# Optimization experiments

Measured on AMD Instinct MI355X. Metric: run time of the kernel, lower is better.

The kernel has to match this reference:

```python
import jax, jax.numpy as jnp
import numpy as np
from jax import lax

DN = ('NCHW', 'OIHW', 'NCHW')

def _bconv(x, w, b):
    # sign-binarized weights, full-precision conv, kernel 3 pad 1 stride 1
    y = lax.conv_general_dilated(x, jnp.sign(w), window_strides=(1, 1),
                                 padding=[(1, 1), (1, 1)], dimension_numbers=DN)
    return y + b[None, :, None, None]

def _maxpool2(x):
    return lax.reduce_window(x, -jnp.inf, lax.max,
                             window_dimensions=(1, 1, 2, 2),
                             window_strides=(1, 1, 2, 2), padding='VALID')

def setup_inputs() -> dict:
    key = jax.random.key(0)
    ks = jax.random.split(key, 11)
    return {
        'x':   jax.random.normal(ks[0], (128, 3, 224, 224), jnp.float32),
        'w1':  jax.random.normal(ks[1], (16, 3, 3, 3), jnp.float32),
        'b1':  jax.random.normal(ks[2], (16,), jnp.float32),
        'w2':  jax.random.normal(ks[3], (32, 16, 3, 3), jnp.float32),
        'b2':  jax.random.normal(ks[4], (32,), jnp.float32),
        'w3':  jax.random.normal(ks[5], (64, 32, 3, 3), jnp.float32),
        'b3':  jax.random.normal(ks[6], (64,), jnp.float32),
        'wf1': jax.random.normal(ks[7], (128, 50176), jnp.float32),
        'bf1': jax.random.normal(ks[8], (128,), jnp.float32),
        'wf2': jax.random.normal(ks[9], (1000, 128), jnp.float32),
        'bf2': jax.random.normal(ks[10], (1000,), jnp.float32),
    }

def reference(x, w1, b1, w2, b2, w3, b3, wf1, bf1, wf2, bf2):
    h = _maxpool2(jax.nn.relu(_bconv(x, w1, b1)))    # [B,16,112,112]
    h = _maxpool2(jax.nn.relu(_bconv(h, w2, b2)))    # [B,32,56,56]
    h = _maxpool2(jax.nn.relu(_bconv(h, w3, b3)))    # [B,64,28,28]
    h = h.reshape(h.shape[0], -1)                    # [B,50176]
    h = jax.nn.relu(h @ jnp.sign(wf1).T + bf1)       # [B,128]
    return h @ jnp.sign(wf2).T + bf2                 # [B,1000]
```

## Files before the change

### kernel.cpp

```cpp
#include <hip/hip_runtime.h>

typedef __attribute__((ext_vector_type(8))) short short8;
typedef __attribute__((ext_vector_type(8), aligned(8))) short short8u;
typedef __attribute__((ext_vector_type(4))) short short4v;
typedef __attribute__((ext_vector_type(4))) float f32x4;
typedef unsigned short ushort;
typedef unsigned int uint;

static __device__ __forceinline__ float sgn(float v) {
    return (v > 0.f) ? 1.f : ((v < 0.f) ? -1.f : 0.f);
}
static __device__ __forceinline__ ushort f2bf(float f) {
    uint u = __builtin_bit_cast(uint, f);
    u += 0x7fffu + ((u >> 16) & 1u);
    return (ushort)(u >> 16);
}
static __device__ __forceinline__ ushort sgn2bf(float v) {
    return (v > 0.f) ? (ushort)0x3F80 : ((v < 0.f) ? (ushort)0xBF80 : (ushort)0);
}

__global__ void pad_zero(ushort* __restrict__ h1p, ushort* __restrict__ h2p) {
    int t = blockIdx.x * 256 + threadIdx.x;
    const short8 z = {};
    if (t < 115712) {
        int b = t / 904, r = t % 904;
        int cell = r >> 1, half = r & 1;
        int y, xx;
        if (cell < 114)      { y = 0;   xx = cell; }
        else if (cell < 228) { y = 113; xx = cell - 114; }
        else { int s = cell - 228; y = 1 + (s >> 1); xx = (s & 1) ? 113 : 0; }
        *(short8*)&h1p[((b * 114 + y) * 114 + xx) * 16 + half * 8] = z;
    } else {
        t -= 115712;
        if (t >= 116736) return;
        int b = t / 912, r = t % 912;
        int cell = r >> 2, qq = r & 3;
        int y, xx;
        if (cell < 58)       { y = 0;  xx = cell; }
        else if (cell < 116) { y = 57; xx = cell - 58; }
        else { int s = cell - 116; y = 1 + (s >> 1); xx = (s & 1) ? 57 : 0; }
        *(short8*)&h2p[((b * 58 + y) * 58 + xx) * 32 + qq * 8] = z;
    }
}

__global__ void wfrag_prep(const float* __restrict__ w2, const float* __restrict__ w3,
                           const float* __restrict__ w1,
                           ushort* __restrict__ f2, ushort* __restrict__ f3,
                           ushort* __restrict__ f1) {
    int t = blockIdx.x * 256 + threadIdx.x;
    if (t < 5120) {
        int j = t & 7, l = (t >> 3) & 63, nc = t >> 9;
        int n = nc & 1, c = nc >> 1;
        int k = c * 32 + ((l >> 4) << 3) + j;
        ushort v = 0;
        if (k < 144) {
            int ky = k / 48, rem = k % 48, kx = rem >> 4, ci = rem & 15;
            int co = n * 16 + (l & 15);
            v = sgn2bf(w2[((co * 16 + ci) * 3 + ky) * 3 + kx]);
        }
        f2[t] = v;
    } else if (t < 23552) {
        int t2 = t - 5120;
        int j = t2 & 7, l = (t2 >> 3) & 63, nc = t2 >> 9;
        int n = nc & 3, c = nc >> 2;
        int k = c * 32 + ((l >> 4) << 3) + j;
        int ky = k / 96, rem = k % 96, kx = rem >> 5, ci = rem & 31;
        int co = n * 16 + (l & 15);
        f3[t2] = sgn2bf(w3[((co * 32 + ci) * 3 + ky) * 3 + kx]);
    } else {
        int t1 = t - 23552;
        if (t1 >= 1024) return;
        int j = t1 & 7, l = (t1 >> 3) & 63, c = t1 >> 9;
        int k = c * 32 + ((l >> 4) << 3) + j;
        int ky = k >> 4, kx = (k >> 2) & 3, ci = k & 3;
        ushort v = 0;
        if (ky < 3 && kx < 3 && ci < 3) {
            int co = l & 15;
            v = sgn2bf(w1[((co * 3 + ci) * 3 + ky) * 3 + kx]);
        }
        f1[t1] = v;
    }
}

__global__ void wf1_prep_t(const float* __restrict__ wf1, ushort* __restrict__ wsg) {
    const int pt  = blockIdx.x;
    const int co2 = blockIdx.y;
    __shared__ ushort T[64][114];
#pragma unroll
    for (int k = 0; k < 7; ++k) {
        int i = threadIdx.x + k * 256;
        int co = i / 28, pf = i % 28;
        const float4 v = *(const float4*)&wf1[(size_t)co2 * 50176 + co * 784 + pt * 112 + pf * 4];
        T[co][pf * 4 + 0] = sgn2bf(v.x);
        T[co][pf * 4 + 1] = sgn2bf(v.y);
        T[co][pf * 4 + 2] = sgn2bf(v.z);
        T[co][pf * 4 + 3] = sgn2bf(v.w);
    }
    __syncthreads();
#pragma unroll
    for (int k = 0; k < 7; ++k) {
        int j = threadIdx.x + k * 256;
        int p = j >> 4, cg = j & 15;
        ushort pk[4] = {T[cg * 4 + 0][p], T[cg * 4 + 1][p], T[cg * 4 + 2][p], T[cg * 4 + 3][p]};
        *(short4v*)&wsg[(size_t)co2 * 50176 + (size_t)(pt * 112 + p) * 64 + cg * 4] =
            *(const short4v*)pk;
    }
}

__global__ __launch_bounds__(256) void
conv1_fused(const float* __restrict__ x,
            const ushort* __restrict__ wfrag,
            const float* __restrict__ bias,
            ushort* __restrict__ h1p) {
    const int py = blockIdx.x;
    const int b  = blockIdx.z;
    const int wv = threadIdx.x >> 6, l = threadIdx.x & 63;

    __shared__ ushort lx[4][232][4];

    {
        const int row = 2 * py - 1 + wv;
        const bool rok = ((unsigned)row < 224u);
        const float* xb = x + (((size_t)b * 3) * 224 + (rok ? row : 0)) * 224;
#pragma unroll
        for (int it = 0; it < 2; ++it) {
            const int cp = l + it * 64;
            if (cp < 112) {
                float2 v0 = {0.f, 0.f}, v1 = {0.f, 0.f}, v2 = {0.f, 0.f};
                if (rok) {
                    v0 = *(const float2*)(xb + 2 * cp);
                    v1 = *(const float2*)(xb + 50176 + 2 * cp);
                    v2 = *(const float2*)(xb + 100352 + 2 * cp);
                }
                ushort pk0[4] = {f2bf(v0.x), f2bf(v1.x), f2bf(v2.x), 0};
                ushort pk1[4] = {f2bf(v0.y), f2bf(v1.y), f2bf(v2.y), 0};
                *(short4v*)&lx[wv][1 + 2 * cp][0] = *(const short4v*)pk0;
                *(short4v*)&lx[wv][2 + 2 * cp][0] = *(const short4v*)pk1;
            }
        }
        if (l == 62) { ushort z[4] = {0,0,0,0}; *(short4v*)&lx[wv][0][0]   = *(const short4v*)z; }
        if (l == 63) { ushort z[4] = {0,0,0,0}; *(short4v*)&lx[wv][225][0] = *(const short4v*)z; }
    }
    __syncthreads();

    const int lhi = l >> 4, llo = l & 15;
    const int q = llo >> 2, e = llo & 3;
    const int xl0 = wv * 56 + 2 * q + (e & 1);
    const int r0  = e >> 1;

    short8 wf[2];
#pragma unroll
    for (int c = 0; c < 2; ++c)
        wf[c] = *(const short8*)&wfrag[(c * 64 + l) * 8];
    const float bv = bias[llo];

    const ushort* lptr[2]; bool vld[2];
#pragma unroll
    for (int c = 0; c < 2; ++c) {
        const int cc = c * 4 + lhi, ky = cc >> 1, half = cc & 1;
        vld[c] = (ky < 3);
        const int kyc = vld[c] ? ky : 0;
        lptr[c] = &lx[r0 + kyc][xl0 + 2 * half][0];
    }

    f32x4 acc[7];
#pragma unroll
    for (int i = 0; i < 7; ++i) acc[i] = (f32x4){0.f, 0.f, 0.f, 0.f};

#pragma unroll
    for (int i = 0; i < 7; ++i)
#pragma unroll
        for (int c = 0; c < 2; ++c) {
            short8 a = {};
            if (vld[c]) a = (short8)(*(const short8u*)(lptr[c] + i * 32));
            acc[i] = __builtin_amdgcn_mfma_f32_16x16x32_bf16(a, wf[c], acc[i], 0, 0, 0);
        }

    const size_t obase = ((size_t)(b * 114 + 1 + py) * 114 + 1) * 16 + llo;
#pragma unroll
    for (int i = 0; i < 7; ++i) {
        float v = fmaxf(fmaxf(acc[i][0], acc[i][1]), fmaxf(acc[i][2], acc[i][3]));
        v = fmaxf(v + bv, 0.f);
        h1p[obase + (size_t)(wv * 28 + i * 4 + lhi) * 16] = f2bf(v);
    }
}

__global__ __launch_bounds__(256, 2) void
conv2_mfma(const ushort* __restrict__ h1p,
           const ushort* __restrict__ wfrag,
           const float* __restrict__ bias,
           ushort* __restrict__ h2p) {
    const int b  = blockIdx.z;
    const int wv = threadIdx.x >> 6, l = threadIdx.x & 63;
    const int mh = wv >> 1, r = wv & 1;
    const int py = blockIdx.x * 2 + r;
    const int lhi = l >> 4, llo = l & 15;
    const int q = llo >> 2, e = llo & 3;
    const int xpre0 = mh * 56 + 2 * q + (e & 1);
    const int ypre  = 2 * py + (e >> 1);

    short8 wf[5][2];
#pragma unroll
    for (int c = 0; c < 5; ++c)
#pragma unroll
        for (int n = 0; n < 2; ++n)
            wf[c][n] = *(const short8*)&wfrag[(((c * 2 + n) * 64) + l) * 8];
    const float bv0 = bias[llo], bv1 = bias[16 + llo];

    const ushort* ptr[5]; bool vld[5];
#pragma unroll
    for (int c = 0; c < 5; ++c) {
        const int cc = c * 4 + lhi;
        vld[c] = (cc < 18);
        const int dy = vld[c] ? (cc / 6) : 0;
        const int koff = (cc % 6) * 8;
        ptr[c] = &h1p[(((size_t)(b * 114 + ypre + dy)) * 114 + xpre0) * 16 + koff];
    }

    f32x4 acc[7][2];
#pragma unroll
    for (int m = 0; m < 7; ++m)
#pragma unroll
        for (int n = 0; n < 2; ++n) acc[m][n] = (f32x4){0.f, 0.f, 0.f, 0.f};

#pragma unroll
    for (int c = 0; c < 5; ++c) {
        short8 a[7];
#pragma unroll
        for (int m = 0; m < 7; ++m) {
            short8 t = {};
            if (vld[c]) t = *(const short8*)(ptr[c] + m * 128);
            a[m] = t;
        }
#pragma unroll
        for (int m = 0; m < 7; ++m) {
            acc[m][0] = __builtin_amdgcn_mfma_f32_16x16x32_bf16(a[m], wf[c][0], acc[m][0], 0, 0, 0);
            acc[m][1] = __builtin_amdgcn_mfma_f32_16x16x32_bf16(a[m], wf[c][1], acc[m][1], 0, 0, 0);
        }
    }

    const size_t obase = ((size_t)(b * 58 + 1 + py) * 58 + 1) * 32 + llo;
#pragma unroll
    for (int m = 0; m < 7; ++m) {
        const size_t po = obase + (size_t)(mh * 28 + m * 4 + lhi) * 32;
        float v0 = fmaxf(fmaxf(acc[m][0][0], acc[m][0][1]), fmaxf(acc[m][0][2], acc[m][0][3]));
        h2p[po]      = f2bf(fmaxf(v0 + bv0, 0.f));
        float v1 = fmaxf(fmaxf(acc[m][1][0], acc[m][1][1]), fmaxf(acc[m][1][2], acc[m][1][3]));
        h2p[po + 16] = f2bf(fmaxf(v1 + bv1, 0.f));
    }
}

__global__ __launch_bounds__(256, 2) void
conv3_mfma(const ushort* __restrict__ h2p,
           const ushort* __restrict__ wfrag,
           const float* __restrict__ bias,
           ushort* __restrict__ h3b) {
    const int b  = blockIdx.z;
    const int wv = threadIdx.x >> 6, l = threadIdx.x & 63;
    const int py = blockIdx.x * 4 + wv;
    const int lhi = l >> 4, llo = l & 15;
    const int q = llo >> 2, e = llo & 3;
    const int xpre0 = 2 * q + (e & 1);
    const int ypre  = 2 * py + (e >> 1);

    const float bv[4] = {bias[llo], bias[16 + llo], bias[32 + llo], bias[48 + llo]};

    const ushort* ptr[9];
#pragma unroll
    for (int c = 0; c < 9; ++c) {
        const int cc = c * 4 + lhi;
        const int dy = cc / 12, koff = (cc % 12) * 8;
        ptr[c] = &h2p[(((size_t)(b * 58 + ypre + dy)) * 58 + xpre0) * 32 + koff];
    }

    f32x4 acc[7][4];
#pragma unroll
    for (int m = 0; m < 7; ++m)
#pragma unroll
        for (int n = 0; n < 4; ++n) acc[m][n] = (f32x4){0.f, 0.f, 0.f, 0.f};

#pragma unroll
    for (int c = 0; c < 9; ++c) {
        const short8 wf0 = *(const short8*)&wfrag[(((c * 4 + 0) * 64) + l) * 8];
        const short8 wf1 = *(const short8*)&wfrag[(((c * 4 + 1) * 64) + l) * 8];
        const short8 wf2 = *(const short8*)&wfrag[(((c * 4 + 2) * 64) + l) * 8];
        const short8 wf3 = *(const short8*)&wfrag[(((c * 4 + 3) * 64) + l) * 8];
        short8 a[7];
#pragma unroll
        for (int m = 0; m < 7; ++m)
            a[m] = *(const short8*)(ptr[c] + m * 256);
#pragma unroll
        for (int m = 0; m < 7; ++m) {
            acc[m][0] = __builtin_amdgcn_mfma_f32_16x16x32_bf16(a[m], wf0, acc[m][0], 0, 0, 0);
            acc[m][1] = __builtin_amdgcn_mfma_f32_16x16x32_bf16(a[m], wf1, acc[m][1], 0, 0, 0);
            acc[m][2] = __builtin_amdgcn_mfma_f32_16x16x32_bf16(a[m], wf2, acc[m][2], 0, 0, 0);
            acc[m][3] = __builtin_amdgcn_mfma_f32_16x16x32_bf16(a[m], wf3, acc[m][3], 0, 0, 0);
        }
    }

    const size_t obase = (size_t)b * 50176 + (size_t)(py * 28) * 64 + llo;
#pragma unroll
    for (int m = 0; m < 7; ++m) {
        const size_t po = obase + (size_t)(m * 4 + lhi) * 64;
#pragma unroll
        for (int n = 0; n < 4; ++n) {
            float v = fmaxf(fmaxf(acc[m][n][0], acc[m][n][1]),
                            fmaxf(acc[m][n][2], acc[m][n][3]));
            v = fmaxf(v + bv[n], 0.f);
            h3b[po + n * 16] = f2bf(v);
        }
    }
}

__global__ __launch_bounds__(256) void
fc1_mfmaA(const ushort* __restrict__ actb,
          const ushort* __restrict__ wsg,
          float* __restrict__ partials) {
    const int K = 50176;
    const int bt = blockIdx.x * 32, ct = blockIdx.y * 32, ks = blockIdx.z;
    const int wv = threadIdx.x >> 6, l = threadIdx.x & 63;
    const int lhi = l >> 4, llo = l & 15;

    __shared__ float lds[4][32][33];

    f32x4 acc[2][2];
#pragma unroll
    for (int i = 0; i < 2; ++i)
#pragma unroll
        for (int j = 0; j < 2; ++j) acc[i][j] = (f32x4){0.f, 0.f, 0.f, 0.f};

    const int kw = ks * 1024 + wv * 256 + lhi * 8;
    const ushort* a0p = actb + (size_t)(bt + llo)      * K + kw;
    const ushort* a1p = actb + (size_t)(bt + llo + 16) * K + kw;
    const ushort* b0p = wsg  + (size_t)(ct + llo)      * K + kw;
    const ushort* b1p = wsg  + (size_t)(ct + llo + 16) * K + kw;

#pragma unroll
    for (int s = 0; s < 8; ++s) {
        const int off = s * 32;
        const short8 a0 = *(const short8*)(a0p + off);
        const short8 a1 = *(const short8*)(a1p + off);
        const short8 b0 = *(const short8*)(b0p + off);
        const short8 b1 = *(const short8*)(b1p + off);
        acc[0][0] = __builtin_amdgcn_mfma_f32_16x16x32_bf16(a0, b0, acc[0][0], 0, 0, 0);
        acc[0][1] = __builtin_amdgcn_mfma_f32_16x16x32_bf16(a0, b1, acc[0][1], 0, 0, 0);
        acc[1][0] = __builtin_amdgcn_mfma_f32_16x16x32_bf16(a1, b0, acc[1][0], 0, 0, 0);
        acc[1][1] = __builtin_amdgcn_mfma_f32_16x16x32_bf16(a1, b1, acc[1][1], 0, 0, 0);
    }

#pragma unroll
    for (int i = 0; i < 2; ++i)
#pragma unroll
        for (int jj = 0; jj < 2; ++jj)
#pragma unroll
            for (int j = 0; j < 4; ++j)
                lds[wv][i * 16 + lhi * 4 + j][jj * 16 + llo] = acc[i][jj][j];
    __syncthreads();

    float* pb = partials + (size_t)ks * 16384;
#pragma unroll
    for (int u = 0; u < 4; ++u) {
        int idx = threadIdx.x + u * 256;
        int m = idx >> 5, n = idx & 31;
        float v = lds[0][m][n] + lds[1][m][n] + lds[2][m][n] + lds[3][m][n];
        pb[(bt + m) * 128 + ct + n] = v;
    }
}

__global__ void fc1_stageB(const float* __restrict__ partials,
                           const float* __restrict__ bf,
                           float* __restrict__ f1) {
    const int o = blockIdx.x * 256 + threadIdx.x;
    float acc = 0.f;
    for (int ks = 0; ks < 49; ++ks) acc += partials[(size_t)ks * 16384 + o];
    f1[o] = fmaxf(acc + bf[o & 127], 0.f);
}

__global__ void fc2_kernel(const float* __restrict__ act,
                           const float* __restrict__ wf,
                           const float* __restrict__ bf,
                           float* __restrict__ out) {
    const int o = blockIdx.x * 256 + threadIdx.x;
    if (o >= 128 * 1000) return;
    const int b = o / 1000, co = o % 1000;
    const float* a  = act + b * 128;
    const float* wr = wf + co * 128;
    float acc = 0.f;
#pragma unroll 8
    for (int k = 0; k < 128; ++k)
        acc = fmaf(a[k], sgn(wr[k]), acc);
    out[o] = acc + bf[co];
}

extern "C" void kernel_launch(void* const* d_in, const int* in_sizes, int n_in,
                              void* d_out, int out_size, void* d_ws, size_t ws_size,
                              hipStream_t stream) {
    const float* x   = (const float*)d_in[0];
    const float* w1  = (const float*)d_in[1];
    const float* b1  = (const float*)d_in[2];
    const float* w2  = (const float*)d_in[3];
    const float* b2  = (const float*)d_in[4];
    const float* w3  = (const float*)d_in[5];
    const float* b3  = (const float*)d_in[6];
    const float* wf1 = (const float*)d_in[7];
    const float* bf1 = (const float*)d_in[8];
    const float* wf2 = (const float*)d_in[9];
    const float* bf2 = (const float*)d_in[10];

    char* ws = (char*)d_ws;
    ushort* h1p  = (ushort*)ws;
    ushort* h3b  = (ushort*)(ws + 53231616u);
    ushort* wsg1 = (ushort*)(ws + 66076672u);
    float*  pa   = (float*) (ws + 78921728u);
    float*  f1   = (float*) (ws + 82132992u);
    ushort* h2p  = (ushort*)(ws + 105507840u);
    ushort* wf1frag = (ushort*)(ws + 133065728u);
    ushort* wf2frag = (ushort*)(ws + 133067776u);
    ushort* wf3frag = (ushort*)(ws + 133078016u);

    pad_zero<<<908, 256, 0, stream>>>(h1p, h2p);
    wfrag_prep<<<96, 256, 0, stream>>>(w2, w3, w1, wf2frag, wf3frag, wf1frag);
    wf1_prep_t<<<dim3(7, 128), 256, 0, stream>>>(wf1, wsg1);
    conv1_fused<<<dim3(112, 1, 128), 256, 0, stream>>>(x, wf1frag, b1, h1p);
    conv2_mfma<<<dim3(28, 1, 128), 256, 0, stream>>>(h1p, wf2frag, b2, h2p);
    conv3_mfma<<<dim3(7, 1, 128), 256, 0, stream>>>(h2p, wf3frag, b3, h3b);
    fc1_mfmaA<<<dim3(4, 4, 49), 256, 0, stream>>>(h3b, wsg1, pa);
    fc1_stageB<<<64, 256, 0, stream>>>(pa, bf1, f1);
    fc2_kernel<<<500, 256, 0, stream>>>(f1, wf2, bf2, (float*)d_out);
}
```

Before: 142.3 us.

## Compute two pooled rows per conv1 block to share halo input rows

Each conv1 block now produces two pooled output rows instead of one. It loads six input rows into shared memory instead of four, so the overlapping halo row loads are reused and fewer redundant input reads and conversions happen. Each wave now covers half the width (14 tiles instead of 7), and all LDS fragment loads are issued before the MFMA chain to expose more load-level parallelism. The grid is halved, which raises per-thread register pressure and lowers the number of blocks.

```diff
diff --git a/kernel.cpp b/kernel.cpp
--- a/kernel.cpp
+++ b/kernel.cpp
@@ -112,14 +112,14 @@
             const ushort* __restrict__ wfrag,
             const float* __restrict__ bias,
             ushort* __restrict__ h1p) {
-    const int py = blockIdx.x;
-    const int b  = blockIdx.z;
+    const int py2 = blockIdx.x;
+    const int b   = blockIdx.z;
     const int wv = threadIdx.x >> 6, l = threadIdx.x & 63;
 
-    __shared__ ushort lx[4][232][4];
-
-    {
-        const int row = 2 * py - 1 + wv;
+    __shared__ ushort lx[6][232][4];
+
+    for (int rr = wv; rr < 6; rr += 4) {
+        const int row = 4 * py2 - 1 + rr;
         const bool rok = ((unsigned)row < 224u);
         const float* xb = x + (((size_t)b * 3) * 224 + (rok ? row : 0)) * 224;
 #pragma unroll
@@ -134,19 +134,20 @@
                 }
                 ushort pk0[4] = {f2bf(v0.x), f2bf(v1.x), f2bf(v2.x), 0};
                 ushort pk1[4] = {f2bf(v0.y), f2bf(v1.y), f2bf(v2.y), 0};
-                *(short4v*)&lx[wv][1 + 2 * cp][0] = *(const short4v*)pk0;
-                *(short4v*)&lx[wv][2 + 2 * cp][0] = *(const short4v*)pk1;
+                *(short4v*)&lx[rr][1 + 2 * cp][0] = *(const short4v*)pk0;
+                *(short4v*)&lx[rr][2 + 2 * cp][0] = *(const short4v*)pk1;
             }
         }
-        if (l == 62) { ushort z[4] = {0,0,0,0}; *(short4v*)&lx[wv][0][0]   = *(const short4v*)z; }
-        if (l == 63) { ushort z[4] = {0,0,0,0}; *(short4v*)&lx[wv][225][0] = *(const short4v*)z; }
+        if (l == 62) { ushort z[4] = {0,0,0,0}; *(short4v*)&lx[rr][0][0]   = *(const short4v*)z; }
+        if (l == 63) { ushort z[4] = {0,0,0,0}; *(short4v*)&lx[rr][225][0] = *(const short4v*)z; }
     }
     __syncthreads();
 
+    const int sr = wv >> 1, hh = wv & 1;
     const int lhi = l >> 4, llo = l & 15;
     const int q = llo >> 2, e = llo & 3;
-    const int xl0 = wv * 56 + 2 * q + (e & 1);
-    const int r0  = e >> 1;
+    const int xl0 = hh * 112 + 2 * q + (e & 1);
+    const int r0  = 2 * sr + (e >> 1);
 
     short8 wf[2];
 #pragma unroll
@@ -163,25 +164,30 @@
         lptr[c] = &lx[r0 + kyc][xl0 + 2 * half][0];
     }
 
-    f32x4 acc[7];
-#pragma unroll
-    for (int i = 0; i < 7; ++i) acc[i] = (f32x4){0.f, 0.f, 0.f, 0.f};
-
-#pragma unroll
-    for (int i = 0; i < 7; ++i)
-#pragma unroll
-        for (int c = 0; c < 2; ++c) {
-            short8 a = {};
-            if (vld[c]) a = (short8)(*(const short8u*)(lptr[c] + i * 32));
-            acc[i] = __builtin_amdgcn_mfma_f32_16x16x32_bf16(a, wf[c], acc[i], 0, 0, 0);
-        }
-
-    const size_t obase = ((size_t)(b * 114 + 1 + py) * 114 + 1) * 16 + llo;
-#pragma unroll
-    for (int i = 0; i < 7; ++i) {
+    f32x4 acc[14];
+#pragma unroll
+    for (int i = 0; i < 14; ++i) acc[i] = (f32x4){0.f, 0.f, 0.f, 0.f};
+
+#pragma unroll
+    for (int c = 0; c < 2; ++c) {
+        short8 a[14];
+#pragma unroll
+        for (int i = 0; i < 14; ++i) {
+            short8 t = {};
+            if (vld[c]) t = (short8)(*(const short8u*)(lptr[c] + i * 32));
+            a[i] = t;
+        }
+#pragma unroll
+        for (int i = 0; i < 14; ++i)
+            acc[i] = __builtin_amdgcn_mfma_f32_16x16x32_bf16(a[i], wf[c], acc[i], 0, 0, 0);
+    }
+
+    const size_t obase = ((size_t)(b * 114 + 1 + 2 * py2 + sr) * 114 + 1) * 16 + llo;
+#pragma unroll
+    for (int i = 0; i < 14; ++i) {
         float v = fmaxf(fmaxf(acc[i][0], acc[i][1]), fmaxf(acc[i][2], acc[i][3]));
         v = fmaxf(v + bv, 0.f);
-        h1p[obase + (size_t)(wv * 28 + i * 4 + lhi) * 16] = f2bf(v);
+        h1p[obase + (size_t)(hh * 56 + i * 4 + lhi) * 16] = f2bf(v);
     }
 }
 
@@ -421,7 +427,7 @@
     pad_zero<<<908, 256, 0, stream>>>(h1p, h2p);
     wfrag_prep<<<96, 256, 0, stream>>>(w2, w3, w1, wf2frag, wf3frag, wf1frag);
     wf1_prep_t<<<dim3(7, 128), 256, 0, stream>>>(wf1, wsg1);
-    conv1_fused<<<dim3(112, 1, 128), 256, 0, stream>>>(x, wf1frag, b1, h1p);
+    conv1_fused<<<dim3(56, 1, 128), 256, 0, stream>>>(x, wf1frag, b1, h1p);
     conv2_mfma<<<dim3(28, 1, 128), 256, 0, stream>>>(h1p, wf2frag, b2, h2p);
     conv3_mfma<<<dim3(7, 1, 128), 256, 0, stream>>>(h2p, wf3frag, b3, h3b);
     fc1_mfmaA<<<dim3(4, 4, 49), 256, 0, stream>>>(h3b, wsg1, pa);
```

Measured after the change: 145.2 us. 2.0% more time.

## Widen fc1 tiles to all 128 outputs and shrink K split chunk

Applied to the files above, without the earlier changes.

The fc1 kernel now computes all 128 output columns per block with a 256-wide K slice, so each activation tile is loaded once instead of four times. The split-K count rises from 49 to 196, which enlarges the partial-sum buffer. The reduction kernel is rewritten with four independent accumulators. This trades duplicated activation loads for more partial-sum traffic, larger LDS use and more register pressure.

```diff
diff --git a/kernel.cpp b/kernel.cpp
--- a/kernel.cpp
+++ b/kernel.cpp
@@ -312,58 +312,62 @@
     }
 }
 
-__global__ __launch_bounds__(256) void
+__global__ __launch_bounds__(256, 2) void
 fc1_mfmaA(const ushort* __restrict__ actb,
           const ushort* __restrict__ wsg,
           float* __restrict__ partials) {
     const int K = 50176;
-    const int bt = blockIdx.x * 32, ct = blockIdx.y * 32, ks = blockIdx.z;
+    const int bt = blockIdx.x * 32, ks = blockIdx.z;
     const int wv = threadIdx.x >> 6, l = threadIdx.x & 63;
     const int lhi = l >> 4, llo = l & 15;
 
-    __shared__ float lds[4][32][33];
-
-    f32x4 acc[2][2];
+    __shared__ float lds[4][32][128];
+
+    f32x4 acc[2][8];
 #pragma unroll
     for (int i = 0; i < 2; ++i)
 #pragma unroll
-        for (int j = 0; j < 2; ++j) acc[i][j] = (f32x4){0.f, 0.f, 0.f, 0.f};
-
-    const int kw = ks * 1024 + wv * 256 + lhi * 8;
+        for (int j = 0; j < 8; ++j) acc[i][j] = (f32x4){0.f, 0.f, 0.f, 0.f};
+
+    const int kw = ks * 256 + wv * 64 + lhi * 8;
     const ushort* a0p = actb + (size_t)(bt + llo)      * K + kw;
     const ushort* a1p = actb + (size_t)(bt + llo + 16) * K + kw;
-    const ushort* b0p = wsg  + (size_t)(ct + llo)      * K + kw;
-    const ushort* b1p = wsg  + (size_t)(ct + llo + 16) * K + kw;
-
-#pragma unroll
-    for (int s = 0; s < 8; ++s) {
+    const ushort* bp[8];
+#pragma unroll
+    for (int j = 0; j < 8; ++j)
+        bp[j] = wsg + (size_t)(j * 16 + llo) * K + kw;
+
+#pragma unroll
+    for (int s = 0; s < 2; ++s) {
         const int off = s * 32;
         const short8 a0 = *(const short8*)(a0p + off);
         const short8 a1 = *(const short8*)(a1p + off);
-        const short8 b0 = *(const short8*)(b0p + off);
-        const short8 b1 = *(const short8*)(b1p + off);
-        acc[0][0] = __builtin_amdgcn_mfma_f32_16x16x32_bf16(a0, b0, acc[0][0], 0, 0, 0);
-        acc[0][1] = __builtin_amdgcn_mfma_f32_16x16x32_bf16(a0, b1, acc[0][1], 0, 0, 0);
-        acc[1][0] = __builtin_amdgcn_mfma_f32_16x16x32_bf16(a1, b0, acc[1][0], 0, 0, 0);
-        acc[1][1] = __builtin_amdgcn_mfma_f32_16x16x32_bf16(a1, b1, acc[1][1], 0, 0, 0);
+        short8 bv[8];
+#pragma unroll
+        for (int j = 0; j < 8; ++j) bv[j] = *(const short8*)(bp[j] + off);
+#pragma unroll
+        for (int j = 0; j < 8; ++j) {
+            acc[0][j] = __builtin_amdgcn_mfma_f32_16x16x32_bf16(a0, bv[j], acc[0][j], 0, 0, 0);
+            acc[1][j] = __builtin_amdgcn_mfma_f32_16x16x32_bf16(a1, bv[j], acc[1][j], 0, 0, 0);
+        }
     }
 
 #pragma unroll
     for (int i = 0; i < 2; ++i)
 #pragma unroll
-        for (int jj = 0; jj < 2; ++jj)
-#pragma unroll
-            for (int j = 0; j < 4; ++j)
-                lds[wv][i * 16 + lhi * 4 + j][jj * 16 + llo] = acc[i][jj][j];
+        for (int j = 0; j < 8; ++j)
+#pragma unroll
+            for (int r = 0; r < 4; ++r)
+                lds[wv][i * 16 + lhi * 4 + r][j * 16 + llo] = acc[i][j][r];
     __syncthreads();
 
     float* pb = partials + (size_t)ks * 16384;
 #pragma unroll
-    for (int u = 0; u < 4; ++u) {
+    for (int u = 0; u < 16; ++u) {
         int idx = threadIdx.x + u * 256;
-        int m = idx >> 5, n = idx & 31;
+        int m = idx >> 7, n = idx & 127;
         float v = lds[0][m][n] + lds[1][m][n] + lds[2][m][n] + lds[3][m][n];
-        pb[(bt + m) * 128 + ct + n] = v;
+        pb[(bt + m) * 128 + n] = v;
     }
 }
 
@@ -371,9 +375,14 @@
                            const float* __restrict__ bf,
                            float* __restrict__ f1) {
     const int o = blockIdx.x * 256 + threadIdx.x;
-    float acc = 0.f;
-    for (int ks = 0; ks < 49; ++ks) acc += partials[(size_t)ks * 16384 + o];
-    f1[o] = fmaxf(acc + bf[o & 127], 0.f);
+    float a0 = 0.f, a1 = 0.f, a2 = 0.f, a3 = 0.f;
+    for (int ks = 0; ks < 196; ks += 4) {
+        a0 += partials[(size_t)(ks + 0) * 16384 + o];
+        a1 += partials[(size_t)(ks + 1) * 16384 + o];
+        a2 += partials[(size_t)(ks + 2) * 16384 + o];
+        a3 += partials[(size_t)(ks + 3) * 16384 + o];
+    }
+    f1[o] = fmaxf((a0 + a1) + (a2 + a3) + bf[o & 127], 0.f);
 }
 
 __global__ void fc2_kernel(const float* __restrict__ act,
@@ -412,7 +421,7 @@
     ushort* h3b  = (ushort*)(ws + 53231616u);
     ushort* wsg1 = (ushort*)(ws + 66076672u);
     float*  pa   = (float*) (ws + 78921728u);
-    float*  f1   = (float*) (ws + 82132992u);
+    float*  f1   = (float*) (ws + 91766784u);
     ushort* h2p  = (ushort*)(ws + 105507840u);
     ushort* wf1frag = (ushort*)(ws + 133065728u);
     ushort* wf2frag = (ushort*)(ws + 133067776u);
@@ -424,7 +433,7 @@
     conv1_fused<<<dim3(112, 1, 128), 256, 0, stream>>>(x, wf1frag, b1, h1p);
     conv2_mfma<<<dim3(28, 1, 128), 256, 0, stream>>>(h1p, wf2frag, b2, h2p);
     conv3_mfma<<<dim3(7, 1, 128), 256, 0, stream>>>(h2p, wf3frag, b3, h3b);
-    fc1_mfmaA<<<dim3(4, 4, 49), 256, 0, stream>>>(h3b, wsg1, pa);
+    fc1_mfmaA<<<dim3(4, 1, 196), 256, 0, stream>>>(h3b, wsg1, pa);
     fc1_stageB<<<64, 256, 0, stream>>>(pa, bf1, f1);
     fc2_kernel<<<500, 256, 0, stream>>>(f1, wf2, bf2, (float*)d_out);
 }
```

Result: slower. 154.3 us (+8.4%).
